# Kernel optimization log

Hardware: AMD Instinct MI355X
Metric: run time of the kernel (lower is better)

## Reference

```python
import jax, jax.numpy as jnp
import numpy as np

I, H, O = 3, 50, 1

def setup_inputs() -> dict:
    key = jax.random.key(0)
    ks = jax.random.split(key, 7)
    B, T = 4096, 512
    s_ih = 1.0 / np.sqrt(H)
    x = jax.random.normal(ks[0], (B, T, I), dtype=jnp.float32)
    W_ih = jax.random.uniform(ks[1], (3 * H, I), jnp.float32, -s_ih, s_ih)
    W_hh = jax.random.uniform(ks[2], (3 * H, H), jnp.float32, -s_ih, s_ih)
    b_ih = jax.random.uniform(ks[3], (3 * H,), jnp.float32, -s_ih, s_ih)
    b_hh = jax.random.uniform(ks[4], (3 * H,), jnp.float32, -s_ih, s_ih)
    W_fc = jax.random.uniform(ks[5], (O, H), jnp.float32, -s_ih, s_ih)
    b_fc = jax.random.uniform(ks[6], (O,), jnp.float32, -s_ih, s_ih)
    return {"x": x, "W_ih": W_ih, "W_hh": W_hh, "b_ih": b_ih, "b_hh": b_hh,
            "W_fc": W_fc, "b_fc": b_fc}

def _gru_last_hidden(x, W_ih, W_hh, b_ih, b_hh):
    # x: [B, T, I]. Precompute input projections for all timesteps (one big GEMM).
    B, T, _ = x.shape
    gi = jnp.einsum('bti,gi->btg', x, W_ih) + b_ih  # [B, T, 3H]
    gi = jnp.moveaxis(gi, 1, 0)  # [T, B, 3H] for scan over time

    W_hr, W_hz, W_hn = W_hh[:H], W_hh[H:2*H], W_hh[2*H:]
    b_hr, b_hz, b_hn = b_hh[:H], b_hh[H:2*H], b_hh[2*H:]

    def step(h, gi_t):
        gir, giz, gin = gi_t[:, :H], gi_t[:, H:2*H], gi_t[:, 2*H:]
        r = jax.nn.sigmoid(gir + h @ W_hr.T + b_hr)
        z = jax.nn.sigmoid(giz + h @ W_hz.T + b_hz)
        n = jnp.tanh(gin + r * (h @ W_hn.T + b_hn))
        h_new = (1.0 - z) * n + z * h
        return h_new, None

    h0 = jnp.zeros((B, H), dtype=x.dtype)
    h_last, _ = jax.lax.scan(step, h0, gi)
    return h_last  # [B, H]

def reference(x, W_ih, W_hh, b_ih, b_hh, W_fc, b_fc):
    h_last = _gru_last_hidden(x, W_ih, W_hh, b_ih, b_hh)
    out = h_last @ W_fc.T + b_fc  # [B, 1]
    return out.squeeze(-1)  # [B]
```

## Files before the change

### kernel.cpp

```cpp
#include <hip/hip_runtime.h>
#include <hip/hip_bf16.h>

#define T_LEN 512
#define HID 50
#define NBATCH 4096

using short8  = __attribute__((ext_vector_type(8))) short;
using floatx4 = __attribute__((ext_vector_type(4))) float;

__device__ __forceinline__ float sigm(float v) {
  return __builtin_amdgcn_rcpf(1.0f + __builtin_amdgcn_exp2f(-1.442695041f * v));
}
__device__ __forceinline__ float tanh_f(float v) {
  return 1.0f - 2.0f * __builtin_amdgcn_rcpf(1.0f + __builtin_amdgcn_exp2f(2.885390082f * v));
}

__device__ __forceinline__ short8 afrag(const char* plane, int rowoff, int off16) {
  return *(const short8*)(plane + rowoff + off16);
}

__global__ __launch_bounds__(256, 1)
void gru_mfma_kernel(const float* __restrict__ x,
                     const float* __restrict__ W_ih,
                     const float* __restrict__ W_hh,
                     const float* __restrict__ b_ih,
                     const float* __restrict__ b_hh,
                     const float* __restrict__ W_fc,
                     const float* __restrict__ b_fc,
                     float* __restrict__ out) {
  __shared__ alignas(16) unsigned char lds[16384];
  char* xs   = (char*)lds;
  char* hbuf = (char*)lds + 12288;

  const int tid  = threadIdx.x;
  const int lane = tid & 63;
  const int w    = tid >> 6;
  const int ucol = lane & 15;
  const int kg   = lane >> 4;
  const int b0   = blockIdx.x * 16;
  const int u    = 16 * w + ucol;
  const bool uv  = (u < HID);

  const float c_r  = uv ? (b_ih[u] + b_hh[u]) : 0.f;
  const float c_z  = uv ? (b_ih[50 + u] + b_hh[50 + u]) : 0.f;
  const float c_ni = uv ? b_ih[100 + u] : 0.f;
  const float c_nh = uv ? b_hh[100 + u] : 0.f;
  float u_r[3], u_z[3], u_n[3];
#pragma unroll
  for (int c = 0; c < 3; ++c) {
    u_r[c] = uv ? W_ih[u * 3 + c] : 0.f;
    u_z[c] = uv ? W_ih[(50 + u) * 3 + c] : 0.f;
    u_n[c] = uv ? W_ih[(100 + u) * 3 + c] : 0.f;
  }
  const float wfc = uv ? W_fc[u] : 0.f;

  short8 Bh[3][2], Bl[3][2];
#pragma unroll
  for (int tau = 0; tau < 3; ++tau) {
    const int row = uv ? (tau * 50 + u) : 0;
    const float* Wrow = W_hh + row * HID;
#pragma unroll
    for (int f = 0; f < 2; ++f) {
      union { short a[8]; short8 s; } ph, pl;
#pragma unroll
      for (int e = 0; e < 8; ++e) {
        const int k = 32 * f + 8 * kg + e;
        const float v = (uv && k < HID) ? Wrow[k] : 0.f;
        __hip_bfloat16 bh = __float2bfloat16(v);
        const float vh = __bfloat162float(bh);
        __hip_bfloat16 bl = __float2bfloat16(v - vh);
        ph.a[e] = *(short*)&bh;
        pl.a[e] = *(short*)&bl;
      }
      Bh[tau][f] = ph.s;
      Bl[tau][f] = pl.s;
    }
  }

  ((float4*)hbuf)[tid] = make_float4(0.f, 0.f, 0.f, 0.f);

  float h[4] = {0.f, 0.f, 0.f, 0.f};

  const int arow = ucol * 128;
  const int axr  = (ucol & 7) << 4;
  const floatx4 z4 = {0.f, 0.f, 0.f, 0.f};

  for (int tc = 0; tc < 8; ++tc) {
    {
      const int sm = tid >> 4, seg = tid & 15;
      const float* xb = x + (size_t)(b0 + sm) * (T_LEN * 3) + tc * 192 + seg * 12;
      const float4 v0 = *(const float4*)(xb + 0);
      const float4 v1 = *(const float4*)(xb + 4);
      const float4 v2 = *(const float4*)(xb + 8);
      const float vv[12] = {v0.x, v0.y, v0.z, v0.w, v1.x, v1.y, v1.z, v1.w, v2.x, v2.y, v2.z, v2.w};
#pragma unroll
      for (int jj = 0; jj < 12; ++jj) {
        const int i = seg * 12 + jj;
        *(float*)(xs + (i / 3) * 192 + (i % 3) * 64 + sm * 4) = vv[jj];
      }
    }
    __syncthreads();

#pragma unroll 2
    for (int s = 0; s < 64; ++s) {
      const int par = s & 1;
      const char* rp = hbuf + par * 2048;
      char*       wp = hbuf + (par ^ 1) * 2048;

      const float4 xv0 = *(const float4*)(xs + s * 192 + 0 * 64 + kg * 16);
      const float4 xv1 = *(const float4*)(xs + s * 192 + 1 * 64 + kg * 16);
      const float4 xv2 = *(const float4*)(xs + s * 192 + 2 * 64 + kg * 16);

      const short8 A0 = afrag(rp, arow, (16 * kg +  0) ^ axr);
      const short8 A1 = afrag(rp, arow, (16 * kg + 64) ^ axr);

      floatx4 accA[3], accB[3];
#pragma unroll
      for (int tau = 0; tau < 3; ++tau) {
        floatx4 a = __builtin_amdgcn_mfma_f32_16x16x32_bf16(A0, Bh[tau][0], z4, 0, 0, 0);
        a = __builtin_amdgcn_mfma_f32_16x16x32_bf16(A1, Bh[tau][1], a, 0, 0, 0);
        accA[tau] = a;
        floatx4 b = __builtin_amdgcn_mfma_f32_16x16x32_bf16(A0, Bl[tau][0], z4, 0, 0, 0);
        b = __builtin_amdgcn_mfma_f32_16x16x32_bf16(A1, Bl[tau][1], b, 0, 0, 0);
        accB[tau] = b;
      }

      const float xa[4]  = {xv0.x, xv0.y, xv0.z, xv0.w};
      const float xb_[4] = {xv1.x, xv1.y, xv1.z, xv1.w};
      const float xc[4]  = {xv2.x, xv2.y, xv2.z, xv2.w};
#pragma unroll
      for (int r = 0; r < 4; ++r) {
        const float x0 = xa[r], x1 = xb_[r], x2 = xc[r];
        const float ar = accA[0][r] + accB[0][r];
        const float az = accA[1][r] + accB[1][r];
        const float an = accA[2][r] + accB[2][r];
        const float gr = fmaf(x0, u_r[0], fmaf(x1, u_r[1], fmaf(x2, u_r[2], c_r)));
        const float gz = fmaf(x0, u_z[0], fmaf(x1, u_z[1], fmaf(x2, u_z[2], c_z)));
        const float gn = fmaf(x0, u_n[0], fmaf(x1, u_n[1], fmaf(x2, u_n[2], c_ni)));
        const float rr = sigm(ar + gr);
        const float zz = sigm(az + gz);
        const float nv = gn + rr * (an + c_nh);
        const float nn = tanh_f(nv);
        const float hn = nn + zz * (h[r] - nn);
        h[r] = hn;
        __hip_bfloat16 bh = __float2bfloat16(hn);
        const int mrow = 4 * kg + r;
        *(unsigned short*)(wp + mrow * 128 + ((2 * u) ^ ((mrow & 7) << 4))) =
            *(const unsigned short*)&bh;
      }
      __syncthreads();
    }
  }

  float p[4];
#pragma unroll
  for (int r = 0; r < 4; ++r) p[r] = h[r] * wfc;
#pragma unroll
  for (int mask = 1; mask < 16; mask <<= 1) {
#pragma unroll
    for (int r = 0; r < 4; ++r) p[r] += __shfl_xor(p[r], mask);
  }
  if (ucol == 0) {
    *(float4*)(lds + (w * 16 + 4 * kg) * 4) = make_float4(p[0], p[1], p[2], p[3]);
  }
  __syncthreads();
  if (tid < 16) {
    float ssum = 0.f;
#pragma unroll
    for (int ww = 0; ww < 4; ++ww) ssum += *(const float*)(lds + (ww * 16 + tid) * 4);
    out[b0 + tid] = ssum + b_fc[0];
  }
}

extern "C" void kernel_launch(void* const* d_in, const int* in_sizes, int n_in,
                              void* d_out, int out_size, void* d_ws, size_t ws_size,
                              hipStream_t stream) {
  const float* x    = (const float*)d_in[0];
  const float* W_ih = (const float*)d_in[1];
  const float* W_hh = (const float*)d_in[2];
  const float* b_ih = (const float*)d_in[3];
  const float* b_hh = (const float*)d_in[4];
  const float* W_fc = (const float*)d_in[5];
  const float* b_fc = (const float*)d_in[6];
  float* out = (float*)d_out;

  dim3 grid(NBATCH / 16);
  dim3 block(256);
  gru_mfma_kernel<<<grid, block, 0, stream>>>(x, W_ih, W_hh, b_ih, b_hh, W_fc, b_fc, out);
}
```

Measured before the change: 248.7 us.

## Fold input projection and biases into MFMA via augmented hidden-state columns

Puts x_t (as hi/lo bf16 parts) and a constant-one column into the unused K slots 50-56 of the hidden-state A matrix. W_ih and the biases go into the matching B fragments, so the input projection and bias adds happen inside the MFMAs instead of as per-step scalar FMAs. The hi/lo accumulations are chained into one accumulator per gate, and a separate aC accumulator carries the n-gate input term. The x for step t+1 is written by wave 3 lanes into the next h buffer, with the x staging loads shifted by one timestep. This trades VALU work for two extra MFMAs and more divergent store logic, and the off-by-one x staging and padding add correctness risk.

```diff
diff --git a/kernel.cpp b/kernel.cpp
--- a/kernel.cpp
+++ b/kernel.cpp
@@ -14,9 +14,12 @@
 __device__ __forceinline__ float tanh_f(float v) {
   return 1.0f - 2.0f * __builtin_amdgcn_rcpf(1.0f + __builtin_amdgcn_exp2f(2.885390082f * v));
 }
-
-__device__ __forceinline__ short8 afrag(const char* plane, int rowoff, int off16) {
-  return *(const short8*)(plane + rowoff + off16);
+__device__ __forceinline__ unsigned short bf16hi(float v) {
+  __hip_bfloat16 b = __float2bfloat16(v);
+  return *(unsigned short*)&b;
+}
+__device__ __forceinline__ float bf16tof(unsigned short u) {
+  return __uint_as_float((unsigned int)u << 16);
 }
 
 __global__ __launch_bounds__(256, 1)
@@ -36,63 +39,114 @@
   const int lane = tid & 63;
   const int w    = tid >> 6;
   const int ucol = lane & 15;
-  const int kg   = lane >> 4;
+  const int kg   = lane >> 6 ? 0 : (lane >> 4);
   const int b0   = blockIdx.x * 16;
   const int u    = 16 * w + ucol;
   const bool uv  = (u < HID);
 
-  const float c_r  = uv ? (b_ih[u] + b_hh[u]) : 0.f;
-  const float c_z  = uv ? (b_ih[50 + u] + b_hh[50 + u]) : 0.f;
-  const float c_ni = uv ? b_ih[100 + u] : 0.f;
-  const float c_nh = uv ? b_hh[100 + u] : 0.f;
-  float u_r[3], u_z[3], u_n[3];
-#pragma unroll
-  for (int c = 0; c < 3; ++c) {
-    u_r[c] = uv ? W_ih[u * 3 + c] : 0.f;
-    u_z[c] = uv ? W_ih[(50 + u) * 3 + c] : 0.f;
-    u_n[c] = uv ? W_ih[(100 + u) * 3 + c] : 0.f;
-  }
   const float wfc = uv ? W_fc[u] : 0.f;
 
   short8 Bh[3][2], Bl[3][2];
-#pragma unroll
-  for (int tau = 0; tau < 3; ++tau) {
-    const int row = uv ? (tau * 50 + u) : 0;
-    const float* Wrow = W_hh + row * HID;
+  short8 Bch, Bcl;
+#pragma unroll
+  for (int g = 0; g < 3; ++g) {
 #pragma unroll
     for (int f = 0; f < 2; ++f) {
       union { short a[8]; short8 s; } ph, pl;
 #pragma unroll
       for (int e = 0; e < 8; ++e) {
         const int k = 32 * f + 8 * kg + e;
-        const float v = (uv && k < HID) ? Wrow[k] : 0.f;
-        __hip_bfloat16 bh = __float2bfloat16(v);
-        const float vh = __bfloat162float(bh);
-        __hip_bfloat16 bl = __float2bfloat16(v - vh);
-        ph.a[e] = *(short*)&bh;
-        pl.a[e] = *(short*)&bl;
-      }
-      Bh[tau][f] = ph.s;
-      Bl[tau][f] = pl.s;
-    }
+        float v = 0.f;
+        if (uv) {
+          if (k < HID) v = W_hh[(g * 50 + u) * HID + k];
+          else if (g < 2) {
+            if (k <= 52)      v = W_ih[(g * 50 + u) * 3 + (k - 50)];
+            else if (k == 53) v = b_ih[g * 50 + u] + b_hh[g * 50 + u];
+            else if (k <= 56) v = W_ih[(g * 50 + u) * 3 + (k - 54)];
+          } else {
+            if (k == 53)      v = b_hh[100 + u];
+          }
+        }
+        const unsigned short hi = bf16hi(v);
+        const unsigned short lo = bf16hi(v - bf16tof(hi));
+        ph.a[e] = (short)hi; pl.a[e] = (short)lo;
+      }
+      Bh[g][f] = ph.s; Bl[g][f] = pl.s;
+    }
+  }
+  {
+    union { short a[8]; short8 s; } ph, pl;
+#pragma unroll
+    for (int e = 0; e < 8; ++e) {
+      const int k = 32 + 8 * kg + e;
+      float v = 0.f;
+      if (uv) {
+        if (k >= 50 && k <= 52)      v = W_ih[(100 + u) * 3 + (k - 50)];
+        else if (k == 53)            v = b_ih[100 + u];
+        else if (k >= 54 && k <= 56) v = W_ih[(100 + u) * 3 + (k - 54)];
+      }
+      const unsigned short hi = bf16hi(v);
+      const unsigned short lo = bf16hi(v - bf16tof(hi));
+      ph.a[e] = (short)hi; pl.a[e] = (short)lo;
+    }
+    Bch = ph.s; Bcl = pl.s;
   }
 
   ((float4*)hbuf)[tid] = make_float4(0.f, 0.f, 0.f, 0.f);
+  __syncthreads();
+  if (tid < 64) {
+    const int m = tid & 15, c = tid >> 4;
+    char* p0 = hbuf + m * 128;
+    const int xr = (m & 7) << 4;
+    if (c == 3) {
+      *(unsigned short*)(p0 + ((2 * 53) ^ xr)) = 0x3F80;
+    } else {
+      const float xv = x[(size_t)(b0 + m) * (T_LEN * 3) + c];
+      const unsigned short hi = bf16hi(xv);
+      const unsigned short lo = bf16hi(xv - bf16tof(hi));
+      *(unsigned short*)(p0 + ((2 * (50 + c)) ^ xr)) = hi;
+      *(unsigned short*)(p0 + ((2 * (54 + c)) ^ xr)) = lo;
+    }
+  }
 
   float h[4] = {0.f, 0.f, 0.f, 0.f};
-
   const int arow = ucol * 128;
   const int axr  = (ucol & 7) << 4;
   const floatx4 z4 = {0.f, 0.f, 0.f, 0.f};
 
+  int hoff[4];
+#pragma unroll
+  for (int r = 0; r < 4; ++r) {
+    const int m = 4 * kg + r;
+    hoff[r] = m * 128 + ((2 * u) ^ ((m & 7) << 4));
+  }
+  int xcomp = 0, xcol = 53;
+  if (ucol >= 2 && ucol <= 4) { xcomp = ucol - 2; xcol = 50 + xcomp; }
+  else if (ucol >= 6 && ucol <= 8) { xcomp = ucol - 6; xcol = 54 + xcomp; }
+  int xoff[4], xroff[4];
+#pragma unroll
+  for (int r = 0; r < 4; ++r) {
+    const int m = 4 * kg + r;
+    xoff[r]  = m * 128 + ((2 * xcol) ^ ((m & 7) << 4));
+    xroff[r] = xcomp * 64 + m * 4;
+  }
+
   for (int tc = 0; tc < 8; ++tc) {
     {
       const int sm = tid >> 4, seg = tid & 15;
-      const float* xb = x + (size_t)(b0 + sm) * (T_LEN * 3) + tc * 192 + seg * 12;
-      const float4 v0 = *(const float4*)(xb + 0);
-      const float4 v1 = *(const float4*)(xb + 4);
-      const float4 v2 = *(const float4*)(xb + 8);
-      const float vv[12] = {v0.x, v0.y, v0.z, v0.w, v1.x, v1.y, v1.z, v1.w, v2.x, v2.y, v2.z, v2.w};
+      const float* xb = x + (size_t)(b0 + sm) * (T_LEN * 3) + tc * 192 + 3 + seg * 12;
+      float vv[12];
+      if (tc == 7 && seg == 15) {
+#pragma unroll
+        for (int j = 0; j < 12; ++j) vv[j] = (j < 9) ? xb[j] : 0.f;
+      } else {
+        const float4 v0 = *(const float4*)(xb + 0);
+        const float4 v1 = *(const float4*)(xb + 4);
+        const float4 v2 = *(const float4*)(xb + 8);
+        vv[0]=v0.x; vv[1]=v0.y; vv[2]=v0.z; vv[3]=v0.w;
+        vv[4]=v1.x; vv[5]=v1.y; vv[6]=v1.z; vv[7]=v1.w;
+        vv[8]=v2.x; vv[9]=v2.y; vv[10]=v2.z; vv[11]=v2.w;
+      }
 #pragma unroll
       for (int jj = 0; jj < 12; ++jj) {
         const int i = seg * 12 + jj;
@@ -107,46 +161,64 @@
       const char* rp = hbuf + par * 2048;
       char*       wp = hbuf + (par ^ 1) * 2048;
 
-      const float4 xv0 = *(const float4*)(xs + s * 192 + 0 * 64 + kg * 16);
-      const float4 xv1 = *(const float4*)(xs + s * 192 + 1 * 64 + kg * 16);
-      const float4 xv2 = *(const float4*)(xs + s * 192 + 2 * 64 + kg * 16);
-
-      const short8 A0 = afrag(rp, arow, (16 * kg +  0) ^ axr);
-      const short8 A1 = afrag(rp, arow, (16 * kg + 64) ^ axr);
-
-      floatx4 accA[3], accB[3];
-#pragma unroll
-      for (int tau = 0; tau < 3; ++tau) {
-        floatx4 a = __builtin_amdgcn_mfma_f32_16x16x32_bf16(A0, Bh[tau][0], z4, 0, 0, 0);
-        a = __builtin_amdgcn_mfma_f32_16x16x32_bf16(A1, Bh[tau][1], a, 0, 0, 0);
-        accA[tau] = a;
-        floatx4 b = __builtin_amdgcn_mfma_f32_16x16x32_bf16(A0, Bl[tau][0], z4, 0, 0, 0);
-        b = __builtin_amdgcn_mfma_f32_16x16x32_bf16(A1, Bl[tau][1], b, 0, 0, 0);
-        accB[tau] = b;
-      }
-
-      const float xa[4]  = {xv0.x, xv0.y, xv0.z, xv0.w};
-      const float xb_[4] = {xv1.x, xv1.y, xv1.z, xv1.w};
-      const float xc[4]  = {xv2.x, xv2.y, xv2.z, xv2.w};
+      const short8 A0 = *(const short8*)(rp + arow + ((16 * kg)      ^ axr));
+      const short8 A1 = *(const short8*)(rp + arow + ((16 * kg + 64) ^ axr));
+
+      floatx4 aR = __builtin_amdgcn_mfma_f32_16x16x32_bf16(A0, Bh[0][0], z4, 0, 0, 0);
+      aR = __builtin_amdgcn_mfma_f32_16x16x32_bf16(A1, Bh[0][1], aR, 0, 0, 0);
+      aR = __builtin_amdgcn_mfma_f32_16x16x32_bf16(A0, Bl[0][0], aR, 0, 0, 0);
+      aR = __builtin_amdgcn_mfma_f32_16x16x32_bf16(A1, Bl[0][1], aR, 0, 0, 0);
+      floatx4 aZ = __builtin_amdgcn_mfma_f32_16x16x32_bf16(A0, Bh[1][0], z4, 0, 0, 0);
+      aZ = __builtin_amdgcn_mfma_f32_16x16x32_bf16(A1, Bh[1][1], aZ, 0, 0, 0);
+      aZ = __builtin_amdgcn_mfma_f32_16x16x32_bf16(A0, Bl[1][0], aZ, 0, 0, 0);
+      aZ = __builtin_amdgcn_mfma_f32_16x16x32_bf16(A1, Bl[1][1], aZ, 0, 0, 0);
+      floatx4 aN = __builtin_amdgcn_mfma_f32_16x16x32_bf16(A0, Bh[2][0], z4, 0, 0, 0);
+      aN = __builtin_amdgcn_mfma_f32_16x16x32_bf16(A1, Bh[2][1], aN, 0, 0, 0);
+      aN = __builtin_amdgcn_mfma_f32_16x16x32_bf16(A0, Bl[2][0], aN, 0, 0, 0);
+      aN = __builtin_amdgcn_mfma_f32_16x16x32_bf16(A1, Bl[2][1], aN, 0, 0, 0);
+      floatx4 aC = __builtin_amdgcn_mfma_f32_16x16x32_bf16(A1, Bch, z4, 0, 0, 0);
+      aC = __builtin_amdgcn_mfma_f32_16x16x32_bf16(A1, Bcl, aC, 0, 0, 0);
+
+      unsigned short hb[4];
 #pragma unroll
       for (int r = 0; r < 4; ++r) {
-        const float x0 = xa[r], x1 = xb_[r], x2 = xc[r];
-        const float ar = accA[0][r] + accB[0][r];
-        const float az = accA[1][r] + accB[1][r];
-        const float an = accA[2][r] + accB[2][r];
-        const float gr = fmaf(x0, u_r[0], fmaf(x1, u_r[1], fmaf(x2, u_r[2], c_r)));
-        const float gz = fmaf(x0, u_z[0], fmaf(x1, u_z[1], fmaf(x2, u_z[2], c_z)));
-        const float gn = fmaf(x0, u_n[0], fmaf(x1, u_n[1], fmaf(x2, u_n[2], c_ni)));
-        const float rr = sigm(ar + gr);
-        const float zz = sigm(az + gz);
-        const float nv = gn + rr * (an + c_nh);
+        const float rr = sigm(aR[r]);
+        const float zz = sigm(aZ[r]);
+        const float nv = fmaf(rr, aN[r], aC[r]);
         const float nn = tanh_f(nv);
-        const float hn = nn + zz * (h[r] - nn);
+        const float hn = fmaf(zz, h[r] - nn, nn);
         h[r] = hn;
-        __hip_bfloat16 bh = __float2bfloat16(hn);
-        const int mrow = 4 * kg + r;
-        *(unsigned short*)(wp + mrow * 128 + ((2 * u) ^ ((mrow & 7) << 4))) =
-            *(const unsigned short*)&bh;
+        hb[r] = bf16hi(hn);
+      }
+
+      if (w < 3) {
+#pragma unroll
+        for (int r = 0; r < 4; ++r)
+          *(unsigned short*)(wp + hoff[r]) = hb[r];
+      } else {
+        if (ucol < 2) {
+#pragma unroll
+          for (int r = 0; r < 4; ++r)
+            *(unsigned short*)(wp + hoff[r]) = hb[r];
+        } else if (ucol <= 8) {
+          if (ucol == 5) {
+#pragma unroll
+            for (int r = 0; r < 4; ++r)
+              *(unsigned short*)(wp + xoff[r]) = 0x3F80;
+          } else if (ucol <= 4) {
+#pragma unroll
+            for (int r = 0; r < 4; ++r) {
+              const float xv = *(const float*)(xs + s * 192 + xroff[r]);
+              *(unsigned short*)(wp + xoff[r]) = bf16hi(xv);
+            }
+          } else {
+#pragma unroll
+            for (int r = 0; r < 4; ++r) {
+              const float xv = *(const float*)(xs + s * 192 + xroff[r]);
+              *(unsigned short*)(wp + xoff[r]) = bf16hi(xv - bf16tof(bf16hi(xv)));
+            }
+          }
+        }
       }
       __syncthreads();
     }
```

New measurement: 312.1 us. 25.5% more time.
